# Optimization experiments

Hardware: AMD Instinct MI355X
Metric: run time of the kernel (lower is better)

## Reference

```python
import jax, jax.numpy as jnp
import numpy as np

NUM_HEADS = 12
LN_EPS = 1e-5


def _layernorm(x, w, b):
    m = jnp.mean(x, axis=-1, keepdims=True)
    v = jnp.mean(jnp.square(x - m), axis=-1, keepdims=True)
    return (x - m) * jax.lax.rsqrt(v + LN_EPS) * w + b


def setup_inputs() -> dict:
    key = jax.random.key(0)
    ks = jax.random.split(key, 6)
    B, N, C, H = 8, 1024, 768, 3072
    s = 0.02
    return {
        "x": jax.random.normal(ks[0], (B, N, C), jnp.float32),
        "ln1_w": jnp.ones((C,), jnp.float32),
        "ln1_b": jnp.zeros((C,), jnp.float32),
        "qkv_w": jax.random.normal(ks[1], (3 * C, C), jnp.float32) * s,
        "qkv_b": jnp.zeros((3 * C,), jnp.float32),
        "proj_w": jax.random.normal(ks[2], (C, C), jnp.float32) * s,
        "proj_b": jnp.zeros((C,), jnp.float32),
        "ln2_w": jnp.ones((C,), jnp.float32),
        "ln2_b": jnp.zeros((C,), jnp.float32),
        "fc1_w": jax.random.normal(ks[3], (H, C), jnp.float32) * s,
        "fc1_b": jnp.zeros((H,), jnp.float32),
        "fc2_w": jax.random.normal(ks[4], (C, H), jnp.float32) * s,
        "fc2_b": jnp.zeros((C,), jnp.float32),
    }


def reference(x, ln1_w, ln1_b, qkv_w, qkv_b, proj_w, proj_b,
              ln2_w, ln2_b, fc1_w, fc1_b, fc2_w, fc2_b):
    B, N, C = x.shape
    H = NUM_HEADS
    d = C // H
    scale = d ** (-0.5)

    # --- attention on norm1(x) (size=None path, dropout rates are 0) ---
    h = _layernorm(x, ln1_w, ln1_b)
    qkv = h @ qkv_w.T + qkv_b                      # [B,N,3C]
    qkv = qkv.reshape(B, N, 3, H, d).transpose(2, 0, 3, 1, 4)  # [3,B,H,N,d]
    q, k, v = qkv[0], qkv[1], qkv[2]
    attn = jnp.einsum('bhqd,bhkd->bhqk', q, k) * scale
    attn = jax.nn.softmax(attn, axis=-1)
    o = jnp.einsum('bhqk,bhkd->bhqd', attn, v)     # [B,H,N,d]
    o = o.transpose(0, 2, 1, 3).reshape(B, N, C)
    x_attn = o @ proj_w.T + proj_b

    # --- residual + MLP ---
    x = x + x_attn
    h2 = _layernorm(x, ln2_w, ln2_b)
    h2 = jax.nn.gelu(h2 @ fc1_w.T + fc1_b, approximate=False)
    x = x + (h2 @ fc2_w.T + fc2_b)
    return x
```

## Files before the change

### kernel.cpp

```cpp
#include <hip/hip_runtime.h>
#include <cmath>

typedef __bf16 bf16;
typedef __bf16 bf16x8 __attribute__((ext_vector_type(8)));
typedef __bf16 bf16x4 __attribute__((ext_vector_type(4)));
typedef __bf16 bf16x2 __attribute__((ext_vector_type(2)));
typedef float floatx4 __attribute__((ext_vector_type(4)));

#define MFMA16(A, B, C) __builtin_amdgcn_mfma_f32_16x16x32_bf16((A), (B), (C), 0, 0, 0)

#define GLDS16(g, l)                                                   \
  __builtin_amdgcn_global_load_lds(                                    \
      (const __attribute__((address_space(1))) void*)(g),              \
      (__attribute__((address_space(3))) void*)(l), 16, 0, 0)

static __device__ __forceinline__ int pack2(float a, float b) {
  bf16x2 t;
  t[0] = (bf16)a;
  t[1] = (bf16)b;
  return __builtin_bit_cast(int, t);
}

__global__ __launch_bounds__(256) void pre_kernel(
    const float* __restrict__ x, const float* __restrict__ g,
    const float* __restrict__ be, bf16* __restrict__ h1,
    const float* __restrict__ s0, bf16* __restrict__ d0, int n0,
    const float* __restrict__ s1, bf16* __restrict__ d1, int n1,
    const float* __restrict__ s2, bf16* __restrict__ d2, int n2,
    const float* __restrict__ s3, bf16* __restrict__ d3, int n3) {
  int bid = blockIdx.x;
  int t = threadIdx.x;
  if (bid < 8192) {
    const float* xr = x + (size_t)bid * 768;
    float v0 = xr[t], v1 = xr[t + 256], v2 = xr[t + 512];
    float s = v0 + v1 + v2;
    float s2 = v0 * v0 + v1 * v1 + v2 * v2;
#pragma unroll
    for (int o = 1; o < 64; o <<= 1) {
      s += __shfl_xor(s, o, 64);
      s2 += __shfl_xor(s2, o, 64);
    }
    __shared__ float red[8];
    int w = t >> 6, lane = t & 63;
    if (lane == 0) { red[w] = s; red[4 + w] = s2; }
    __syncthreads();
    float ts = red[0] + red[1] + red[2] + red[3];
    float ts2 = red[4] + red[5] + red[6] + red[7];
    float mean = ts * (1.0f / 768.0f);
    float var = ts2 * (1.0f / 768.0f) - mean * mean;
    float rstd = rsqrtf(var + 1e-5f);
    bf16* orow = h1 + (size_t)bid * 768;
    orow[t]       = (bf16)((v0 - mean) * rstd * g[t]       + be[t]);
    orow[t + 256] = (bf16)((v1 - mean) * rstd * g[t + 256] + be[t + 256]);
    orow[t + 512] = (bf16)((v2 - mean) * rstd * g[t + 512] + be[t + 512]);
    return;
  }
  int i = (bid - 8192) * 256 + t;
  const float* s;
  bf16* d;
  if (i < n0) { s = s0 + (size_t)i * 4; d = d0 + (size_t)i * 4; }
  else if ((i -= n0) < n1) { s = s1 + (size_t)i * 4; d = d1 + (size_t)i * 4; }
  else if ((i -= n1) < n2) { s = s2 + (size_t)i * 4; d = d2 + (size_t)i * 4; }
  else if ((i -= n2) < n3) { s = s3 + (size_t)i * 4; d = d3 + (size_t)i * 4; }
  else return;
  bf16x4 v;
  v[0] = (bf16)s[0]; v[1] = (bf16)s[1]; v[2] = (bf16)s[2]; v[3] = (bf16)s[3];
  *(bf16x4*)d = v;
}

__global__ __launch_bounds__(256) void ln_kernel(const float* __restrict__ x,
                                                 const float* __restrict__ g,
                                                 const float* __restrict__ be,
                                                 bf16* __restrict__ out) {
  int row = blockIdx.x;
  int t = threadIdx.x;
  const float* xr = x + (size_t)row * 768;
  float v0 = xr[t], v1 = xr[t + 256], v2 = xr[t + 512];
  float s = v0 + v1 + v2;
  float s2 = v0 * v0 + v1 * v1 + v2 * v2;
#pragma unroll
  for (int o = 1; o < 64; o <<= 1) {
    s += __shfl_xor(s, o, 64);
    s2 += __shfl_xor(s2, o, 64);
  }
  __shared__ float red[8];
  int w = t >> 6, lane = t & 63;
  if (lane == 0) { red[w] = s; red[4 + w] = s2; }
  __syncthreads();
  float ts = red[0] + red[1] + red[2] + red[3];
  float ts2 = red[4] + red[5] + red[6] + red[7];
  float mean = ts * (1.0f / 768.0f);
  float var = ts2 * (1.0f / 768.0f) - mean * mean;
  float rstd = rsqrtf(var + 1e-5f);
  bf16* orow = out + (size_t)row * 768;
  orow[t]       = (bf16)((v0 - mean) * rstd * g[t]       + be[t]);
  orow[t + 256] = (bf16)((v1 - mean) * rstd * g[t + 256] + be[t + 256]);
  orow[t + 512] = (bf16)((v2 - mean) * rstd * g[t + 512] + be[t + 512]);
}

constexpr int EP_BF16 = 0;
constexpr int EP_RES_F32 = 1;
constexpr int EP_GELU_BF16 = 2;

template <int EP, int NJ>
__global__ __launch_bounds__(256, 3) void gemm_bt(
    const bf16* __restrict__ A, const bf16* __restrict__ Bw,
    const float* __restrict__ bias, const float* __restrict__ resid,
    void* __restrict__ outp, int M, int N, int K) {
  __shared__ alignas(16) bf16 Asl[128 * 64];
  __shared__ alignas(16) bf16 Bsl[NJ * 32 * 64];
  int tid = threadIdx.x;
  int lane = tid & 63, w = tid >> 6;
  int wm = w >> 1, wn = w & 1;
  int q16 = lane & 15, quad = lane >> 4;
  int fid = blockIdx.x + gridDim.x * blockIdx.y;
  int nb = gridDim.x;
  int s = fid >> 3;
  int m0 = ((fid & 7) * (gridDim.y >> 3) + s / nb) * 128;
  int n0 = (s % nb) * (NJ * 32);

  floatx4 acc[4][NJ];
#pragma unroll
  for (int i = 0; i < 4; i++)
#pragma unroll
    for (int j = 0; j < NJ; j++) acc[i][j] = (floatx4){0.f, 0.f, 0.f, 0.f};

  int rIn = lane >> 3;
  int cg = (lane & 7) ^ rIn;
  const bf16* ag[4];
  const bf16* bg[NJ];
#pragma unroll
  for (int q = 0; q < 4; q++)
    ag[q] = A + (size_t)(m0 + (w * 4 + q) * 8 + rIn) * K + cg * 8;
#pragma unroll
  for (int q = 0; q < NJ; q++)
    bg[q] = Bw + (size_t)(n0 + (w * NJ + q) * 8 + rIn) * K + cg * 8;
  bf16* la = &Asl[w * 2048];
  bf16* lb = &Bsl[w * NJ * 512];

  int msel = q16 & 7;
  int offA[2][4], offB[2][NJ];
#pragma unroll
  for (int ks = 0; ks < 2; ks++) {
#pragma unroll
    for (int i = 0; i < 4; i++)
      offA[ks][i] = (wm * 64 + i * 16 + q16) * 64 + (((ks * 4 + quad) ^ msel)) * 8;
#pragma unroll
    for (int j = 0; j < NJ; j++)
      offB[ks][j] = (wn * 16 * NJ + j * 16 + q16) * 64 + (((ks * 4 + quad) ^ msel)) * 8;
  }

  for (int k0 = 0; k0 < K; k0 += 64) {
    __syncthreads();
#pragma unroll
    for (int q = 0; q < 4; q++) {
      GLDS16(ag[q], la + q * 512);
      ag[q] += 64;
    }
#pragma unroll
    for (int q = 0; q < NJ; q++) {
      GLDS16(bg[q], lb + q * 512);
      bg[q] += 64;
    }
    __syncthreads();
#pragma unroll
    for (int ks = 0; ks < 2; ks++) {
      bf16x8 af[4], bfr[NJ];
#pragma unroll
      for (int i = 0; i < 4; i++) af[i] = *(const bf16x8*)&Asl[offA[ks][i]];
#pragma unroll
      for (int j = 0; j < NJ; j++) bfr[j] = *(const bf16x8*)&Bsl[offB[ks][j]];
#pragma unroll
      for (int i = 0; i < 4; i++)
#pragma unroll
        for (int j = 0; j < NJ; j++) acc[i][j] = MFMA16(af[i], bfr[j], acc[i][j]);
    }
  }

#pragma unroll
  for (int i = 0; i < 4; i++) {
#pragma unroll
    for (int j = 0; j < NJ; j++) {
#pragma unroll
      for (int r = 0; r < 4; r++) {
        int m = m0 + wm * 64 + i * 16 + quad * 4 + r;
        int n = n0 + wn * 16 * NJ + j * 16 + q16;
        size_t idx = (size_t)m * N + n;
        float v = acc[i][j][r] + bias[n];
        if constexpr (EP == EP_BF16) {
          ((bf16*)outp)[idx] = (bf16)v;
        } else if constexpr (EP == EP_RES_F32) {
          ((float*)outp)[idx] = v + resid[idx];
        } else {
          float u = v * (2.3022083f + 0.1029443f * v * v);
          float e = __builtin_amdgcn_exp2f(-u);
          float gv = v * __builtin_amdgcn_rcpf(1.0f + e);
          ((bf16*)outp)[idx] = (bf16)gv;
        }
      }
    }
  }
}

__global__ __launch_bounds__(128, 3) void attn_kernel(const bf16* __restrict__ qkv,
                                                      bf16* __restrict__ o) {
  __shared__ alignas(16) bf16 Kl[2][32 * 64];
  __shared__ alignas(16) bf16 Vt[2][64 * 40];
  int tid = threadIdx.x;
  int lane = tid & 63, w = tid >> 6;
  int q16 = lane & 15, quad = lane >> 4;
  int b = blockIdx.y / 12, h = blockIdx.y % 12;
  int qbase = blockIdx.x * 64 + w * 32;
  const int KS = 32 * 2304;

  bf16x8 qf[2][2];
#pragma unroll
  for (int qt = 0; qt < 2; qt++)
#pragma unroll
    for (int c = 0; c < 2; c++)
      qf[qt][c] = *(const bf16x8*)(qkv +
          (size_t)(b * 1024 + qbase + qt * 16 + q16) * 2304 + h * 64 +
          c * 32 + quad * 8);

  int krow = lane >> 3;
  int kchunk = (lane & 7) ^ krow;
  const bf16* kg0 = qkv + (size_t)(b * 1024 + w * 16 + krow) * 2304 + 768 +
                    h * 64 + kchunk * 8;
  const bf16* kg1 = kg0 + 8 * 2304;
  bf16* kdA[2] = {&Kl[0][w * 1024], &Kl[1][w * 1024]};

  int kr = tid >> 2;
  int dbase = (tid & 3) * 16;
  const bf16* vgA = qkv + (size_t)(b * 1024 + kr) * 2304 + 1536 + h * 64 + dbase;
  const bf16* vgB = vgA + 8;
  int vtA[8], vtB[8];
#pragma unroll
  for (int e = 0; e < 8; e++) {
    int dA = dbase + e;
    int dB = dbase + 8 + e;
    vtA[e] = ((dA * 5 + (kr >> 3)) ^ ((dA >> 3) & 7)) * 8 + (kr & 7);
    vtB[e] = ((dB * 5 + (kr >> 3)) ^ ((dB >> 3) & 7)) * 8 + (kr & 7);
  }

  int koff[2][2];
#pragma unroll
  for (int nc = 0; nc < 2; nc++)
#pragma unroll
    for (int ck = 0; ck < 2; ck++) {
      int key = nc * 16 + q16;
      koff[nc][ck] = (key * 8 + ((ck * 4 + quad) ^ (key & 7))) * 8;
    }
  int voff[4];
#pragma unroll
  for (int dc = 0; dc < 4; dc++) {
    int d = dc * 16 + q16;
    voff[dc] = ((d * 5 + quad) ^ ((d >> 3) & 7)) * 8;
  }

  int srcLo = q16 + ((quad & 1) << 5);
  int srcHi = srcLo + 16;
  bool loH = quad < 2;

  float lsum[2] = {0.f, 0.f};
  floatx4 oacc[2][4];
#pragma unroll
  for (int qt = 0; qt < 2; qt++)
#pragma unroll
    for (int dc = 0; dc < 4; dc++) oacc[qt][dc] = (floatx4){0.f, 0.f, 0.f, 0.f};

  GLDS16(kg0, kdA[0]);
  GLDS16(kg1, kdA[0] + 512);
  kg0 += KS; kg1 += KS;
  bf16x8 va = *(const bf16x8*)vgA;
  bf16x8 vb = *(const bf16x8*)vgB;
  vgA += KS; vgB += KS;
#pragma unroll
  for (int e = 0; e < 8; e++) Vt[0][vtA[e]] = va[e];
#pragma unroll
  for (int e = 0; e < 8; e++) Vt[0][vtB[e]] = vb[e];
  va = *(const bf16x8*)vgA;
  vb = *(const bf16x8*)vgB;
  vgA += KS; vgB += KS;

  for (int kt = 0; kt < 32; kt++) {
    int cur = kt & 1, nxt = cur ^ 1;
    __syncthreads();
    if (kt < 31) {
      GLDS16(kg0, kdA[nxt]);
      GLDS16(kg1, kdA[nxt] + 512);
      kg0 += KS; kg1 += KS;
#pragma unroll
      for (int e = 0; e < 8; e++) Vt[nxt][vtA[e]] = va[e];
#pragma unroll
      for (int e = 0; e < 8; e++) Vt[nxt][vtB[e]] = vb[e];
      if (kt < 30) {
        va = *(const bf16x8*)vgA;
        vb = *(const bf16x8*)vgB;
        vgA += KS; vgB += KS;
      }
    }

    bf16x8 kf[2][2];
#pragma unroll
    for (int nc = 0; nc < 2; nc++)
#pragma unroll
      for (int ck = 0; ck < 2; ck++)
        kf[nc][ck] = *(const bf16x8*)&Kl[cur][koff[nc][ck]];
    bf16x8 vf[4];
#pragma unroll
    for (int dc = 0; dc < 4; dc++) vf[dc] = *(const bf16x8*)&Vt[cur][voff[dc]];

#pragma unroll
    for (int qt = 0; qt < 2; qt++) {
      floatx4 z0 = (floatx4){0.f, 0.f, 0.f, 0.f};
      floatx4 z1 = (floatx4){0.f, 0.f, 0.f, 0.f};
      z0 = MFMA16(kf[0][0], qf[qt][0], z0);
      z0 = MFMA16(kf[0][1], qf[qt][1], z0);
      z1 = MFMA16(kf[1][0], qf[qt][0], z1);
      z1 = MFMA16(kf[1][1], qf[qt][1], z1);
      float e0[4], e1[4];
#pragma unroll
      for (int r = 0; r < 4; r++) {
        e0[r] = __builtin_amdgcn_exp2f(z0[r] * 0.18033688011f);
        e1[r] = __builtin_amdgcn_exp2f(z1[r] * 0.18033688011f);
        lsum[qt] += e0[r] + e1[r];
      }
      int A0 = pack2(e0[0], e0[1]);
      int A1 = pack2(e0[2], e0[3]);
      int B0 = pack2(e1[0], e1[1]);
      int B1 = pack2(e1[2], e1[3]);
      int tA0 = __shfl(A0, srcLo, 64), tB0 = __shfl(B0, srcLo, 64);
      int tA1 = __shfl(A1, srcLo, 64), tB1 = __shfl(B1, srcLo, 64);
      int tA2 = __shfl(A0, srcHi, 64), tB2 = __shfl(B0, srcHi, 64);
      int tA3 = __shfl(A1, srcHi, 64), tB3 = __shfl(B1, srcHi, 64);
      union { int i[4]; bf16x8 v; } pu;
      pu.i[0] = loH ? tA0 : tB0;
      pu.i[1] = loH ? tA1 : tB1;
      pu.i[2] = loH ? tA2 : tB2;
      pu.i[3] = loH ? tA3 : tB3;
#pragma unroll
      for (int dc = 0; dc < 4; dc++)
        oacc[qt][dc] = MFMA16(pu.v, vf[dc], oacc[qt][dc]);
    }
  }

#pragma unroll
  for (int qt = 0; qt < 2; qt++) {
    float s = lsum[qt];
    s += __shfl_xor(s, 16, 64);
    s += __shfl_xor(s, 32, 64);
    float inv = 1.0f / s;
    bf16* op = o + (size_t)(b * 1024 + qbase + qt * 16) * 768 + h * 64;
#pragma unroll
    for (int r = 0; r < 4; r++) {
      float invr = __shfl(inv, quad * 4 + r, 64);
#pragma unroll
      for (int dc = 0; dc < 4; dc++)
        op[(size_t)(quad * 4 + r) * 768 + dc * 16 + q16] =
            (bf16)(oacc[qt][dc][r] * invr);
    }
  }
}

extern "C" void kernel_launch(void* const* d_in, const int* in_sizes, int n_in,
                              void* d_out, int out_size, void* d_ws, size_t ws_size,
                              hipStream_t stream) {
  (void)in_sizes; (void)n_in; (void)out_size; (void)ws_size;
  const float* x      = (const float*)d_in[0];
  const float* ln1_w  = (const float*)d_in[1];
  const float* ln1_b  = (const float*)d_in[2];
  const float* qkv_w  = (const float*)d_in[3];
  const float* qkv_b  = (const float*)d_in[4];
  const float* proj_w = (const float*)d_in[5];
  const float* proj_b = (const float*)d_in[6];
  const float* ln2_w  = (const float*)d_in[7];
  const float* ln2_b  = (const float*)d_in[8];
  const float* fc1_w  = (const float*)d_in[9];
  const float* fc1_b  = (const float*)d_in[10];
  const float* fc2_w  = (const float*)d_in[11];
  const float* fc2_b  = (const float*)d_in[12];

  char* ws = (char*)d_ws;
  size_t off = 0;
  auto alloc = [&](size_t bytes) {
    void* p = ws + off;
    off += (bytes + 255) & ~(size_t)255;
    return p;
  };
  bf16* wq  = (bf16*)alloc((size_t)2304 * 768 * 2);
  bf16* wp  = (bf16*)alloc((size_t)768 * 768 * 2);
  bf16* wf1 = (bf16*)alloc((size_t)3072 * 768 * 2);
  bf16* wf2 = (bf16*)alloc((size_t)768 * 3072 * 2);
  bf16* slotA = (bf16*)alloc((size_t)8192 * 768 * 2);
  bf16* slotB = (bf16*)alloc((size_t)8192 * 3072 * 2);
  float* x1 = (float*)alloc((size_t)8192 * 768 * 4);

  bf16* h1 = slotA;
  bf16* qkvb = slotB;
  bf16* ob = slotA;
  bf16* h2 = slotA;
  bf16* hm = slotB;

  pre_kernel<<<8192 + 6912, 256, 0, stream>>>(
      x, ln1_w, ln1_b, h1,
      qkv_w, wq, 2304 * 768 / 4, proj_w, wp, 768 * 768 / 4,
      fc1_w, wf1, 3072 * 768 / 4, fc2_w, wf2, 768 * 3072 / 4);

  gemm_bt<EP_BF16, 4><<<dim3(18, 64), 256, 0, stream>>>(
      h1, wq, qkv_b, nullptr, qkvb, 8192, 2304, 768);
  attn_kernel<<<dim3(16, 96), 128, 0, stream>>>(qkvb, ob);
  gemm_bt<EP_RES_F32, 2><<<dim3(12, 64), 256, 0, stream>>>(
      ob, wp, proj_b, x, x1, 8192, 768, 768);
  ln_kernel<<<8192, 256, 0, stream>>>(x1, ln2_w, ln2_b, h2);
  gemm_bt<EP_GELU_BF16, 4><<<dim3(24, 64), 256, 0, stream>>>(
      h2, wf1, fc1_b, nullptr, hm, 8192, 3072, 768);
  gemm_bt<EP_RES_F32, 2><<<dim3(12, 64), 256, 0, stream>>>(
      hm, wf2, fc2_b, x1, (float*)d_out, 8192, 768, 3072);
}
```

Before: 341.3 us.

## Triple-buffer GEMM LDS with async prefetch and a smaller K-tile

New measurement: 368.4 us. +7.9%, slower.

```diff
diff --git a/kernel.cpp b/kernel.cpp
--- a/kernel.cpp
+++ b/kernel.cpp
@@ -107,8 +107,9 @@
     const bf16* __restrict__ A, const bf16* __restrict__ Bw,
     const float* __restrict__ bias, const float* __restrict__ resid,
     void* __restrict__ outp, int M, int N, int K) {
-  __shared__ alignas(16) bf16 Asl[128 * 64];
-  __shared__ alignas(16) bf16 Bsl[NJ * 32 * 64];
+  __shared__ alignas(16) bf16 Asl[3][128 * 32];
+  __shared__ alignas(16) bf16 Bsl[3][NJ * 32 * 32];
+  constexpr int BB = NJ / 2;
   int tid = threadIdx.x;
   int lane = tid & 63, w = tid >> 6;
   int wm = w >> 1, wn = w & 1;
@@ -125,56 +126,72 @@
 #pragma unroll
     for (int j = 0; j < NJ; j++) acc[i][j] = (floatx4){0.f, 0.f, 0.f, 0.f};
 
-  int rIn = lane >> 3;
-  int cg = (lane & 7) ^ rIn;
-  const bf16* ag[4];
-  const bf16* bg[NJ];
-#pragma unroll
-  for (int q = 0; q < 4; q++)
-    ag[q] = A + (size_t)(m0 + (w * 4 + q) * 8 + rIn) * K + cg * 8;
-#pragma unroll
-  for (int q = 0; q < NJ; q++)
-    bg[q] = Bw + (size_t)(n0 + (w * NJ + q) * 8 + rIn) * K + cg * 8;
-  bf16* la = &Asl[w * 2048];
-  bf16* lb = &Bsl[w * NJ * 512];
-
-  int msel = q16 & 7;
-  int offA[2][4], offB[2][NJ];
-#pragma unroll
-  for (int ks = 0; ks < 2; ks++) {
+  int rL = lane >> 2;
+  int gL = (lane & 3) ^ ((lane >> 3) & 3);
+  const bf16* ag[2];
+#pragma unroll
+  for (int q = 0; q < 2; q++)
+    ag[q] = A + (size_t)(m0 + w * 32 + q * 16 + rL) * K + gL * 8;
+  const bf16* bg[BB];
+#pragma unroll
+  for (int q = 0; q < BB; q++)
+    bg[q] = Bw + (size_t)(n0 + w * (16 * BB) + q * 16 + rL) * K + gL * 8;
+
+  auto stage = [&](int buf) {
+#pragma unroll
+    for (int q = 0; q < 2; q++) {
+      GLDS16(ag[q], &Asl[buf][w * 1024 + q * 512]);
+      ag[q] += 32;
+    }
+#pragma unroll
+    for (int q = 0; q < BB; q++) {
+      GLDS16(bg[q], &Bsl[buf][w * (512 * BB) + q * 512]);
+      bg[q] += 32;
+    }
+  };
+
+  int sw = (q16 >> 1) & 3;
+  int offA[4], offB[NJ];
+#pragma unroll
+  for (int i = 0; i < 4; i++)
+    offA[i] = (wm * 64 + i * 16 + q16) * 32 + ((quad ^ sw) * 8);
+#pragma unroll
+  for (int j = 0; j < NJ; j++)
+    offB[j] = (wn * 16 * NJ + j * 16 + q16) * 32 + ((quad ^ sw) * 8);
+
+  stage(0);
+  stage(1);
+
+  int nT = K >> 5;
+  int cur = 0;
+  for (int t = 0; t < nT; t++) {
+    if (t < nT - 1) {
+      if constexpr (NJ == 4) {
+        asm volatile("s_waitcnt vmcnt(4)" ::: "memory");
+      } else {
+        asm volatile("s_waitcnt vmcnt(3)" ::: "memory");
+      }
+    } else {
+      asm volatile("s_waitcnt vmcnt(0)" ::: "memory");
+    }
+    asm volatile("s_barrier" ::: "memory");
+    if (t + 2 < nT) {
+      int pb = cur + 2;
+      if (pb >= 3) pb -= 3;
+      stage(pb);
+    }
+    const bf16* ab = Asl[cur];
+    const bf16* bb = Bsl[cur];
+    bf16x8 af[4], bfr[NJ];
+#pragma unroll
+    for (int i = 0; i < 4; i++) af[i] = *(const bf16x8*)&ab[offA[i]];
+#pragma unroll
+    for (int j = 0; j < NJ; j++) bfr[j] = *(const bf16x8*)&bb[offB[j]];
 #pragma unroll
     for (int i = 0; i < 4; i++)
-      offA[ks][i] = (wm * 64 + i * 16 + q16) * 64 + (((ks * 4 + quad) ^ msel)) * 8;
-#pragma unroll
-    for (int j = 0; j < NJ; j++)
-      offB[ks][j] = (wn * 16 * NJ + j * 16 + q16) * 64 + (((ks * 4 + quad) ^ msel)) * 8;
-  }
-
-  for (int k0 = 0; k0 < K; k0 += 64) {
-    __syncthreads();
-#pragma unroll
-    for (int q = 0; q < 4; q++) {
-      GLDS16(ag[q], la + q * 512);
-      ag[q] += 64;
-    }
-#pragma unroll
-    for (int q = 0; q < NJ; q++) {
-      GLDS16(bg[q], lb + q * 512);
-      bg[q] += 64;
-    }
-    __syncthreads();
-#pragma unroll
-    for (int ks = 0; ks < 2; ks++) {
-      bf16x8 af[4], bfr[NJ];
-#pragma unroll
-      for (int i = 0; i < 4; i++) af[i] = *(const bf16x8*)&Asl[offA[ks][i]];
-#pragma unroll
-      for (int j = 0; j < NJ; j++) bfr[j] = *(const bf16x8*)&Bsl[offB[ks][j]];
-#pragma unroll
-      for (int i = 0; i < 4; i++)
-#pragma unroll
-        for (int j = 0; j < NJ; j++) acc[i][j] = MFMA16(af[i], bfr[j], acc[i][j]);
-    }
+#pragma unroll
+      for (int j = 0; j < NJ; j++) acc[i][j] = MFMA16(af[i], bfr[j], acc[i][j]);
+    cur = (cur == 2) ? 0 : cur + 1;
   }
 
 #pragma unroll
```

## Enlarge attention tiles to 128 queries and 64 keys per step

Applied to the files above, without the earlier changes.

After: 343.4 us. About the same (+0.6%).

```diff
diff --git a/kernel.cpp b/kernel.cpp
--- a/kernel.cpp
+++ b/kernel.cpp
@@ -202,16 +202,16 @@
   }
 }
 
-__global__ __launch_bounds__(128, 3) void attn_kernel(const bf16* __restrict__ qkv,
+__global__ __launch_bounds__(256, 3) void attn_kernel(const bf16* __restrict__ qkv,
                                                       bf16* __restrict__ o) {
-  __shared__ alignas(16) bf16 Kl[2][32 * 64];
-  __shared__ alignas(16) bf16 Vt[2][64 * 40];
+  __shared__ alignas(16) bf16 Kl[2][64 * 64];
+  __shared__ alignas(16) bf16 Vt[2][64 * 72];
   int tid = threadIdx.x;
   int lane = tid & 63, w = tid >> 6;
   int q16 = lane & 15, quad = lane >> 4;
   int b = blockIdx.y / 12, h = blockIdx.y % 12;
-  int qbase = blockIdx.x * 64 + w * 32;
-  const int KS = 32 * 2304;
+  int qbase = blockIdx.x * 128 + w * 32;
+  const int KS = 64 * 2304;
 
   bf16x8 qf[2][2];
 #pragma unroll
@@ -238,24 +238,26 @@
   for (int e = 0; e < 8; e++) {
     int dA = dbase + e;
     int dB = dbase + 8 + e;
-    vtA[e] = ((dA * 5 + (kr >> 3)) ^ ((dA >> 3) & 7)) * 8 + (kr & 7);
-    vtB[e] = ((dB * 5 + (kr >> 3)) ^ ((dB >> 3) & 7)) * 8 + (kr & 7);
-  }
-
-  int koff[2][2];
-#pragma unroll
-  for (int nc = 0; nc < 2; nc++)
+    vtA[e] = ((dA * 9 + (kr >> 3)) ^ ((dA >> 3) & 7)) * 8 + (kr & 7);
+    vtB[e] = ((dB * 9 + (kr >> 3)) ^ ((dB >> 3) & 7)) * 8 + (kr & 7);
+  }
+
+  int koff[4][2];
+#pragma unroll
+  for (int nc = 0; nc < 4; nc++)
 #pragma unroll
     for (int ck = 0; ck < 2; ck++) {
       int key = nc * 16 + q16;
       koff[nc][ck] = (key * 8 + ((ck * 4 + quad) ^ (key & 7))) * 8;
     }
-  int voff[4];
-#pragma unroll
-  for (int dc = 0; dc < 4; dc++) {
-    int d = dc * 16 + q16;
-    voff[dc] = ((d * 5 + quad) ^ ((d >> 3) & 7)) * 8;
-  }
+  int voff[2][4];
+#pragma unroll
+  for (int c = 0; c < 2; c++)
+#pragma unroll
+    for (int dc = 0; dc < 4; dc++) {
+      int d = dc * 16 + q16;
+      voff[c][dc] = ((d * 9 + (c * 4 + quad)) ^ ((d >> 3) & 7)) * 8;
+    }
 
   int srcLo = q16 + ((quad & 1) << 5);
   int srcHi = srcLo + 16;
@@ -282,10 +284,10 @@
   vb = *(const bf16x8*)vgB;
   vgA += KS; vgB += KS;
 
-  for (int kt = 0; kt < 32; kt++) {
+  for (int kt = 0; kt < 16; kt++) {
     int cur = kt & 1, nxt = cur ^ 1;
     __syncthreads();
-    if (kt < 31) {
+    if (kt < 15) {
       GLDS16(kg0, kdA[nxt]);
       GLDS16(kg1, kdA[nxt] + 512);
       kg0 += KS; kg1 += KS;
@@ -293,54 +295,67 @@
       for (int e = 0; e < 8; e++) Vt[nxt][vtA[e]] = va[e];
 #pragma unroll
       for (int e = 0; e < 8; e++) Vt[nxt][vtB[e]] = vb[e];
-      if (kt < 30) {
+      if (kt < 14) {
         va = *(const bf16x8*)vgA;
         vb = *(const bf16x8*)vgB;
         vgA += KS; vgB += KS;
       }
     }
 
-    bf16x8 kf[2][2];
-#pragma unroll
-    for (int nc = 0; nc < 2; nc++)
-#pragma unroll
-      for (int ck = 0; ck < 2; ck++)
-        kf[nc][ck] = *(const bf16x8*)&Kl[cur][koff[nc][ck]];
-    bf16x8 vf[4];
-#pragma unroll
-    for (int dc = 0; dc < 4; dc++) vf[dc] = *(const bf16x8*)&Vt[cur][voff[dc]];
+    floatx4 z[2][4];
+#pragma unroll
+    for (int nc = 0; nc < 4; nc++) {
+      bf16x8 k0 = *(const bf16x8*)&Kl[cur][koff[nc][0]];
+      bf16x8 k1 = *(const bf16x8*)&Kl[cur][koff[nc][1]];
+#pragma unroll
+      for (int qt = 0; qt < 2; qt++) {
+        floatx4 t = (floatx4){0.f, 0.f, 0.f, 0.f};
+        t = MFMA16(k0, qf[qt][0], t);
+        t = MFMA16(k1, qf[qt][1], t);
+        z[qt][nc] = t;
+      }
+    }
+
+    bf16x8 vf[2][4];
+#pragma unroll
+    for (int c = 0; c < 2; c++)
+#pragma unroll
+      for (int dc = 0; dc < 4; dc++)
+        vf[c][dc] = *(const bf16x8*)&Vt[cur][voff[c][dc]];
 
 #pragma unroll
     for (int qt = 0; qt < 2; qt++) {
-      floatx4 z0 = (floatx4){0.f, 0.f, 0.f, 0.f};
-      floatx4 z1 = (floatx4){0.f, 0.f, 0.f, 0.f};
-      z0 = MFMA16(kf[0][0], qf[qt][0], z0);
-      z0 = MFMA16(kf[0][1], qf[qt][1], z0);
-      z1 = MFMA16(kf[1][0], qf[qt][0], z1);
-      z1 = MFMA16(kf[1][1], qf[qt][1], z1);
-      float e0[4], e1[4];
-#pragma unroll
-      for (int r = 0; r < 4; r++) {
-        e0[r] = __builtin_amdgcn_exp2f(z0[r] * 0.18033688011f);
-        e1[r] = __builtin_amdgcn_exp2f(z1[r] * 0.18033688011f);
-        lsum[qt] += e0[r] + e1[r];
-      }
-      int A0 = pack2(e0[0], e0[1]);
-      int A1 = pack2(e0[2], e0[3]);
-      int B0 = pack2(e1[0], e1[1]);
-      int B1 = pack2(e1[2], e1[3]);
-      int tA0 = __shfl(A0, srcLo, 64), tB0 = __shfl(B0, srcLo, 64);
-      int tA1 = __shfl(A1, srcLo, 64), tB1 = __shfl(B1, srcLo, 64);
-      int tA2 = __shfl(A0, srcHi, 64), tB2 = __shfl(B0, srcHi, 64);
-      int tA3 = __shfl(A1, srcHi, 64), tB3 = __shfl(B1, srcHi, 64);
-      union { int i[4]; bf16x8 v; } pu;
-      pu.i[0] = loH ? tA0 : tB0;
-      pu.i[1] = loH ? tA1 : tB1;
-      pu.i[2] = loH ? tA2 : tB2;
-      pu.i[3] = loH ? tA3 : tB3;
-#pragma unroll
-      for (int dc = 0; dc < 4; dc++)
-        oacc[qt][dc] = MFMA16(pu.v, vf[dc], oacc[qt][dc]);
+      float e_[4][4];
+#pragma unroll
+      for (int nc = 0; nc < 4; nc++)
+#pragma unroll
+        for (int r = 0; r < 4; r++) {
+          e_[nc][r] = __builtin_amdgcn_exp2f(z[qt][nc][r] * 0.18033688011f);
+          lsum[qt] += e_[nc][r];
+        }
+      int P[4][2];
+#pragma unroll
+      for (int nc = 0; nc < 4; nc++) {
+        P[nc][0] = pack2(e_[nc][0], e_[nc][1]);
+        P[nc][1] = pack2(e_[nc][2], e_[nc][3]);
+      }
+      union { int i[4]; bf16x8 v; } pu[2];
+#pragma unroll
+      for (int c = 0; c < 2; c++) {
+        int a0 = __shfl(P[2 * c][0], srcLo, 64), b0 = __shfl(P[2 * c + 1][0], srcLo, 64);
+        int a1 = __shfl(P[2 * c][1], srcLo, 64), b1 = __shfl(P[2 * c + 1][1], srcLo, 64);
+        int a2 = __shfl(P[2 * c][0], srcHi, 64), b2 = __shfl(P[2 * c + 1][0], srcHi, 64);
+        int a3 = __shfl(P[2 * c][1], srcHi, 64), b3 = __shfl(P[2 * c + 1][1], srcHi, 64);
+        pu[c].i[0] = loH ? a0 : b0;
+        pu[c].i[1] = loH ? a1 : b1;
+        pu[c].i[2] = loH ? a2 : b2;
+        pu[c].i[3] = loH ? a3 : b3;
+      }
+#pragma unroll
+      for (int dc = 0; dc < 4; dc++) {
+        oacc[qt][dc] = MFMA16(pu[0].v, vf[0][dc], oacc[qt][dc]);
+        oacc[qt][dc] = MFMA16(pu[1].v, vf[1][dc], oacc[qt][dc]);
+      }
     }
   }
 
@@ -408,7 +423,7 @@
 
   gemm_bt<EP_BF16, 4><<<dim3(18, 64), 256, 0, stream>>>(
       h1, wq, qkv_b, nullptr, qkvb, 8192, 2304, 768);
-  attn_kernel<<<dim3(16, 96), 128, 0, stream>>>(qkvb, ob);
+  attn_kernel<<<dim3(8, 96), 256, 0, stream>>>(qkvb, ob);
   gemm_bt<EP_RES_F32, 2><<<dim3(12, 64), 256, 0, stream>>>(
       ob, wp, proj_b, x, x1, 8192, 768, 768);
   ln_kernel<<<8192, 256, 0, stream>>>(x1, ln2_w, ln2_b, h2);
```
